# Performance work log

Measured on AMD Instinct MI355X. Metric: run time of the kernel, lower is better.

The kernel has to match this reference:

```python
import jax, jax.numpy as jnp
import numpy as np

N = 100000
E = 1600000
NEG_SLOPE = 0.2


def _param(key, shape, scale=0.05):
    return jax.random.normal(key, shape, dtype=jnp.float32) * scale


def setup_inputs() -> dict:
    key = jax.random.key(0)
    ks = jax.random.split(key, 16)
    x = jax.random.normal(ks[0], (N, 128), dtype=jnp.float32)
    edge_index = jax.random.randint(ks[1], (2, E), 0, N, dtype=jnp.int64)
    # layer 1: 128 -> (H=2, C=64), concat
    W1 = _param(ks[2], (128, 2 * 64)); a_src1 = _param(ks[3], (2, 64)); a_dst1 = _param(ks[4], (2, 64)); b1 = jnp.zeros((128,), jnp.float32)
    # layer 2: 128 -> (H=2, C=64), concat
    W2 = _param(ks[5], (128, 2 * 64)); a_src2 = _param(ks[6], (2, 64)); a_dst2 = _param(ks[7], (2, 64)); b2 = jnp.zeros((128,), jnp.float32)
    # layer 3: 128 -> (H=1, C=64), mean (concat=False)
    W3 = _param(ks[8], (128, 1 * 64)); a_src3 = _param(ks[9], (1, 64)); a_dst3 = _param(ks[10], (1, 64)); b3 = jnp.zeros((64,), jnp.float32)
    return {"x": x, "edge_index": edge_index,
            "W1": W1, "a_src1": a_src1, "a_dst1": a_dst1, "b1": b1,
            "W2": W2, "a_src2": a_src2, "a_dst2": a_dst2, "b2": b2,
            "W3": W3, "a_src3": a_src3, "a_dst3": a_dst3, "b3": b3}


def gat_layer(x, src, dst, W, a_src, a_dst, b, concat):
    H, C = a_src.shape
    n = x.shape[0]
    h = (x @ W).reshape(n, H, C)                      # [N,H,C]
    # per-node attention logits (avoid [E,H,C] gather for the score step)
    al_s = jnp.sum(h * a_src[None], axis=-1)          # [N,H]
    al_d = jnp.sum(h * a_dst[None], axis=-1)          # [N,H]
    e = al_s[src] + al_d[dst]                         # [E',H]
    e = jnp.where(e > 0, e, NEG_SLOPE * e)            # LeakyReLU(0.2)
    # scatter-softmax over incoming edges per destination node
    m = jax.ops.segment_max(e, dst, num_segments=n)   # [N,H]
    ex = jnp.exp(e - m[dst])
    z = jax.ops.segment_sum(ex, dst, num_segments=n)  # [N,H]
    alpha = ex / z[dst]                               # [E',H]
    msg = h[src] * alpha[:, :, None]                  # [E',H,C]
    out = jax.ops.segment_sum(msg, dst, num_segments=n)  # [N,H,C]
    out = out.reshape(n, H * C) if concat else out.mean(axis=1)
    return out + b


def reference(x, edge_index, W1, a_src1, a_dst1, b1, W2, a_src2, a_dst2, b2, W3, a_src3, a_dst3, b3):
    n = x.shape[0]
    loop = jnp.arange(n, dtype=edge_index.dtype)
    src = jnp.concatenate([edge_index[0], loop])      # add self-loops (PyG default)
    dst = jnp.concatenate([edge_index[1], loop])
    h = gat_layer(x, src, dst, W1, a_src1, a_dst1, b1, True)
    h = jax.nn.relu(h)
    h = gat_layer(h, src, dst, W2, a_src2, a_dst2, b2, True)
    h = jax.nn.relu(h)
    return gat_layer(h, src, dst, W3, a_src3, a_dst3, b3, False)
```

## Files before the change

kernel.cpp:

```cpp
#include <hip/hip_runtime.h>
#include <hip/hip_bf16.h>

#define NEG_SLOPE 0.2f
#define BUK_SHIFT 9
#define BUK_SIZE 512
#define BUK_CAP 16384

typedef unsigned short u16;
typedef __attribute__((ext_vector_type(8))) short s8v;
typedef __attribute__((ext_vector_type(4))) float f4v;
typedef _Float16 h8 __attribute__((ext_vector_type(8)));

__device__ __forceinline__ u16 f2bf(float v) {
    unsigned u = __float_as_uint(v);
    unsigned r = u + 0x7FFFu + ((u >> 16) & 1u);
    return (u16)(r >> 16);
}
__device__ __forceinline__ float bf2f(u16 h) { return __uint_as_float(((unsigned)h) << 16); }


__global__ void k_zero(int* g_cnt, int nb) {
    int i = blockIdx.x * blockDim.x + threadIdx.x;
    if (i < nb) g_cnt[i] = 0;
}

__launch_bounds__(256)
__global__ void k_binscatter(const int* __restrict__ ei, int* g_cnt, int* buckets,
                             int E, int nb) {
    __shared__ int lcnt[256], lbase[256], lcur[256];
    int t = threadIdx.x;
    if (t < nb) {
        lcnt[t] = 0;
        lcur[t] = 0;
    }
    __syncthreads();
    int tile0 = blockIdx.x * 4096;
    int pk[16], bk[16];
#pragma unroll
    for (int k = 0; k < 16; k++) {
        int idx = tile0 + k * 256 + t;
        bk[k] = -1;
        if (idx < E) {
            int s = ei[idx];
            int d = ei[E + idx];
            bk[k] = d >> BUK_SHIFT;
            pk[k] = (s << BUK_SHIFT) | (d & (BUK_SIZE - 1));
            atomicAdd(&lcnt[bk[k]], 1);
        }
    }
    __syncthreads();
    if (t < nb && lcnt[t] > 0) lbase[t] = atomicAdd(&g_cnt[t], lcnt[t]);
    __syncthreads();
#pragma unroll
    for (int k = 0; k < 16; k++) {
        if (bk[k] >= 0) {
            int p = lbase[bk[k]] + atomicAdd(&lcur[bk[k]], 1);
            if (p < BUK_CAP) buckets[(bk[k] << 14) + p] = pk[k];
        }
    }
}

__launch_bounds__(512)
__global__ void k_csr(const int* __restrict__ g_cnt, const int* __restrict__ buckets,
                      int* csr_ptr, int* csr_src, int n, int nb) {
    __shared__ int lcnt[512], lsc[512], lcur[512], bsc[512];
    int b = blockIdx.x;
    int t = threadIdx.x;
    int nodes = min(BUK_SIZE, n - b * BUK_SIZE);
    int cnt = min(g_cnt[b], BUK_CAP);
    const int* bp = &buckets[b << 14];

    int bv = 0;
    if (t < nb) bv = min(g_cnt[t], BUK_CAP) + min(BUK_SIZE, n - t * BUK_SIZE);
    bsc[t] = bv;
    __syncthreads();
    for (int off = 1; off < 512; off <<= 1) {
        int x = (t >= off) ? bsc[t - off] : 0;
        __syncthreads();
        bsc[t] += x;
        __syncthreads();
    }
    int boff = bsc[b] - (cnt + nodes);
    int total = bsc[nb - 1];
    __syncthreads();

    lcnt[t] = 0;
    __syncthreads();
    for (int i = t; i < cnt; i += 512) atomicAdd(&lcnt[bp[i] & (BUK_SIZE - 1)], 1);
    __syncthreads();
    int myc = (t < nodes) ? (lcnt[t] + 1) : 0;
    lsc[t] = myc;
    __syncthreads();
    for (int off = 1; off < 512; off <<= 1) {
        int x = (t >= off) ? lsc[t - off] : 0;
        __syncthreads();
        lsc[t] += x;
        __syncthreads();
    }
    int excl = lsc[t] - myc;
    lcur[t] = excl;
    if (t < nodes) csr_ptr[b * BUK_SIZE + t] = boff + excl;
    if (b == nb - 1 && t == 0) csr_ptr[n] = total;
    __syncthreads();
    for (int i = t; i < cnt; i += 512) {
        int v = bp[i];
        int ld = v & (BUK_SIZE - 1);
        int p = atomicAdd(&lcur[ld], 1);
        csr_src[boff + p] = v >> BUK_SHIFT;
    }
    if (t < nodes) {
        int p = atomicAdd(&lcur[t], 1);
        csr_src[boff + p] = b * BUK_SIZE + t;
    }
}


__global__ void k_wsplit_all(const float* __restrict__ W1, const float* __restrict__ W2,
                             const float* __restrict__ W3, u16* __restrict__ T1h,
                             u16* __restrict__ T1l, u16* __restrict__ T2h,
                             u16* __restrict__ T2l, u16* __restrict__ T3h,
                             u16* __restrict__ T3l) {
    int t = blockIdx.x * 256 + threadIdx.x;
    const float* W;
    u16 *Th, *Tl;
    int M, idx;
    if (t < 16384) {
        W = W1; Th = T1h; Tl = T1l; M = 128; idx = t;
    } else if (t < 32768) {
        W = W2; Th = T2h; Tl = T2l; M = 128; idx = t - 16384;
    } else if (t < 40960) {
        W = W3; Th = T3h; Tl = T3l; M = 64; idx = t - 32768;
    } else {
        return;
    }
    int c = idx >> 7, k = idx & 127;
    float v = W[(size_t)k * M + c];
    u16 h = f2bf(v);
    u16 l = f2bf(v - bf2f(h));
    int ct = c >> 4, ch = k >> 5, q = (k >> 3) & 3, j = k & 7;
    size_t addr = ((size_t)ct * 4 + ch) * 512 + ((c & 15) + 16 * q) * 8 + j;
    Th[addr] = h;
    Tl[addr] = l;
}


__device__ __forceinline__ void load_split_f32(const float* __restrict__ X, int row,
                                               int koff, int N, s8v& hi, s8v& lo) {
    float v[8];
    if (row < N) {
        float4 a = *(const float4*)&X[(size_t)row * 128 + koff];
        float4 b = *(const float4*)&X[(size_t)row * 128 + koff + 4];
        v[0] = a.x; v[1] = a.y; v[2] = a.z; v[3] = a.w;
        v[4] = b.x; v[5] = b.y; v[6] = b.z; v[7] = b.w;
    } else {
#pragma unroll
        for (int i = 0; i < 8; i++) v[i] = 0.f;
    }
    union { s8v s; u16 u[8]; } H, L;
#pragma unroll
    for (int i = 0; i < 8; i++) {
        H.u[i] = f2bf(v[i]);
        L.u[i] = f2bf(v[i] - bf2f(H.u[i]));
    }
    hi = H.s;
    lo = L.s;
}

template <int M, bool FP32X>
__launch_bounds__(256)
__global__ void k_gemm_mfma(const float* __restrict__ Xf, const u16* __restrict__ XH,
                            const u16* __restrict__ XL, const u16* __restrict__ WTh,
                            const u16* __restrict__ WTl, const float* __restrict__ asrc,
                            const float* __restrict__ adst, _Float16* __restrict__ Hout,
                            float* __restrict__ als, float* __restrict__ ald, int nrows) {
    const int CT = M / 16;
    const int H = (M == 128) ? 2 : 1;
    int tid = threadIdx.x;
    int wv = tid >> 6, lane = tid & 63;
    int q = lane >> 4, nl = lane & 15;
    int R0 = blockIdx.x * 128 + wv * 32;
    int rt0 = R0 >> 4;

    f4v acc[2][CT];
    f4v z4 = {0.f, 0.f, 0.f, 0.f};
#pragma unroll
    for (int rt = 0; rt < 2; rt++)
#pragma unroll
        for (int ct = 0; ct < CT; ct++) acc[rt][ct] = z4;

#pragma unroll
    for (int ch = 0; ch < 4; ch++) {
        s8v ah0, al0, ah1, al1;
        if (FP32X) {
            int koff = ch * 32 + q * 8;
            load_split_f32(Xf, R0 + nl, koff, nrows, ah0, al0);
            load_split_f32(Xf, R0 + 16 + nl, koff, nrows, ah1, al1);
        } else {
            size_t a0 = ((size_t)rt0 * 4 + ch) * 512 + lane * 8;
            size_t a1 = ((size_t)(rt0 + 1) * 4 + ch) * 512 + lane * 8;
            ah0 = *(const s8v*)&XH[a0];
            al0 = *(const s8v*)&XL[a0];
            ah1 = *(const s8v*)&XH[a1];
            al1 = *(const s8v*)&XL[a1];
        }
#pragma unroll
        for (int ct = 0; ct < CT; ct++) {
            size_t bb = ((size_t)ct * 4 + ch) * 512 + lane * 8;
            s8v bh = *(const s8v*)&WTh[bb];
            s8v bl = *(const s8v*)&WTl[bb];
            acc[0][ct] = __builtin_amdgcn_mfma_f32_16x16x32_bf16(ah0, bh, acc[0][ct], 0, 0, 0);
            acc[0][ct] = __builtin_amdgcn_mfma_f32_16x16x32_bf16(ah0, bl, acc[0][ct], 0, 0, 0);
            acc[0][ct] = __builtin_amdgcn_mfma_f32_16x16x32_bf16(al0, bh, acc[0][ct], 0, 0, 0);
            acc[1][ct] = __builtin_amdgcn_mfma_f32_16x16x32_bf16(ah1, bh, acc[1][ct], 0, 0, 0);
            acc[1][ct] = __builtin_amdgcn_mfma_f32_16x16x32_bf16(ah1, bl, acc[1][ct], 0, 0, 0);
            acc[1][ct] = __builtin_amdgcn_mfma_f32_16x16x32_bf16(al1, bh, acc[1][ct], 0, 0, 0);
        }
    }

    float av[CT], dvv[CT];
#pragma unroll
    for (int ct = 0; ct < CT; ct++) {
        av[ct] = asrc[ct * 16 + nl];
        dvv[ct] = adst[ct * 16 + nl];
    }
    float ps[2][4][2], pd[2][4][2];
#pragma unroll
    for (int rt = 0; rt < 2; rt++)
#pragma unroll
        for (int r = 0; r < 4; r++)
            for (int h = 0; h < 2; h++) ps[rt][r][h] = pd[rt][r][h] = 0.f;
#pragma unroll
    for (int rt = 0; rt < 2; rt++)
#pragma unroll
        for (int ct = 0; ct < CT; ct++) {
            int h = (M == 128) ? (ct >> 2) : 0;
#pragma unroll
            for (int r = 0; r < 4; r++) {
                ps[rt][r][h] = fmaf(acc[rt][ct][r], av[ct], ps[rt][r][h]);
                pd[rt][r][h] = fmaf(acc[rt][ct][r], dvv[ct], pd[rt][r][h]);
            }
        }

#pragma unroll
    for (int rt = 0; rt < 2; rt++)
#pragma unroll
        for (int ct = 0; ct < CT; ct++)
#pragma unroll
            for (int r = 0; r < 4; r++) {
                int row = R0 + rt * 16 + q * 4 + r;
                if (row < nrows) Hout[(size_t)row * M + ct * 16 + nl] = (_Float16)acc[rt][ct][r];
            }

#pragma unroll
    for (int rt = 0; rt < 2; rt++)
#pragma unroll
        for (int r = 0; r < 4; r++)
#pragma unroll
            for (int h = 0; h < H; h++) {
                float v1 = ps[rt][r][h], v2 = pd[rt][r][h];
                for (int m = 1; m <= 8; m <<= 1) {
                    v1 += __shfl_xor(v1, m);
                    v2 += __shfl_xor(v2, m);
                }
                int row = R0 + rt * 16 + q * 4 + r;
                if (nl == 0 && row < nrows) {
                    als[(size_t)row * H + h] = v1;
                    ald[(size_t)row * H + h] = v2;
                }
            }
}


__launch_bounds__(256)
__global__ void k_agg128(const int* __restrict__ ptr, const int* __restrict__ srcv,
                         const _Float16* __restrict__ Hh, const float* __restrict__ als,
                         const float* __restrict__ ald, const float* __restrict__ bias,
                         u16* __restrict__ OutH, u16* __restrict__ OutL, int n) {
    int wid = (blockIdx.x * blockDim.x + threadIdx.x) >> 6;
    int lane = threadIdx.x & 63;
    if (wid >= n) return;
    int start = ptr[wid], end = ptr[wid + 1];
    float2 adv = *(const float2*)&ald[(size_t)wid * 2];
    int grp = lane >> 4;
    int gl = lane & 15;
    int hsel = gl >> 3;
    float z0 = 0.f, z1 = 0.f;
    float acc[8];
#pragma unroll
    for (int c = 0; c < 8; c++) acc[c] = 0.f;

    for (int base = start; base < end; base += 64) {
        int i = base + lane;
        int s_l = 0;
        float ex0 = 0.f, ex1 = 0.f;
        if (i < end) {
            s_l = srcv[i];
            float2 av = *(const float2*)&als[(size_t)s_l * 2];
            float e0 = av.x + adv.x;
            e0 = e0 > 0.f ? e0 : NEG_SLOPE * e0;
            ex0 = __expf(e0);
            float e1 = av.y + adv.y;
            e1 = e1 > 0.f ? e1 : NEG_SLOPE * e1;
            ex1 = __expf(e1);
        }
        z0 += ex0;
        z1 += ex1;
        int cntj = min(64, end - base);
        for (int jp = 0; jp < cntj; jp += 16) {
            int nk = min(4, (cntj - jp + 3) >> 2);
            h8 hv[4];
            float w[4];
#pragma unroll
            for (int k = 0; k < 4; k++) {
                if (k < nk) {
                    int j = jp + 4 * k + grp;
                    int s = __shfl(s_l, j);
                    float w0 = __shfl(ex0, j);
                    float w1 = __shfl(ex1, j);
                    w[k] = hsel ? w1 : w0;
                    hv[k] = *(const h8*)&Hh[(size_t)s * 128 + gl * 8];
                }
            }
#pragma unroll
            for (int k = 0; k < 4; k++) {
                if (k < nk) {
#pragma unroll
                    for (int c = 0; c < 8; c++)
                        acc[c] = fmaf(w[k], (float)hv[k][c], acc[c]);
                }
            }
        }
    }

#pragma unroll
    for (int c = 0; c < 8; c++) {
        acc[c] += __shfl_xor(acc[c], 16);
        acc[c] += __shfl_xor(acc[c], 32);
    }
    for (int m = 32; m >= 1; m >>= 1) {
        z0 += __shfl_xor(z0, m);
        z1 += __shfl_xor(z1, m);
    }
    if (lane < 16) {
        float zinv = hsel ? (1.f / z1) : (1.f / z0);
        int c0 = gl * 8;
        float4 b0 = *(const float4*)&bias[c0];
        float4 b1 = *(const float4*)&bias[c0 + 4];
        float bb[8] = {b0.x, b0.y, b0.z, b0.w, b1.x, b1.y, b1.z, b1.w};
        union { u16 u[8]; s8v v; } HH, LL;
#pragma unroll
        for (int c = 0; c < 8; c++) {
            float o = fmaxf(fmaf(acc[c], zinv, bb[c]), 0.f);
            u16 h = f2bf(o);
            HH.u[c] = h;
            LL.u[c] = f2bf(o - bf2f(h));
        }
        int ch = c0 >> 5, qq = (c0 >> 3) & 3;
        size_t tb = ((size_t)(wid >> 4) * 4 + ch) * 512 + ((size_t)((wid & 15) + 16 * qq)) * 8;
        *(s8v*)&OutH[tb] = HH.v;
        *(s8v*)&OutL[tb] = LL.v;
    }
}


__launch_bounds__(256)
__global__ void k_agg64(const int* __restrict__ ptr, const int* __restrict__ srcv,
                        const _Float16* __restrict__ Hh, const float* __restrict__ als,
                        const float* __restrict__ ald, const float* __restrict__ bias,
                        float* __restrict__ Out, int n) {
    int wid = blockIdx.x * 4 + (threadIdx.x >> 6);
    int lane = threadIdx.x & 63;
    if (wid >= n) return;
    int start = ptr[wid], end = ptr[wid + 1];
    float ad0 = ald[wid];
    int grp = lane >> 3;
    int gl = lane & 7;
    float z = 0.f;
    float acc[8];
#pragma unroll
    for (int c = 0; c < 8; c++) acc[c] = 0.f;

    for (int base = start; base < end; base += 64) {
        int i = base + lane;
        int s_l = 0;
        float ex0 = 0.f;
        if (i < end) {
            s_l = srcv[i];
            float e = als[s_l] + ad0;
            e = e > 0.f ? e : NEG_SLOPE * e;
            ex0 = __expf(e);
        }
        z += ex0;
        int cntj = min(64, end - base);
        for (int jp = 0; jp < cntj; jp += 32) {
            int nk = min(4, (cntj - jp + 7) >> 3);
            h8 hv[4];
            float w[4];
#pragma unroll
            for (int k = 0; k < 4; k++) {
                if (k < nk) {
                    int j = jp + 8 * k + grp;
                    int s = __shfl(s_l, j);
                    w[k] = __shfl(ex0, j);
                    hv[k] = *(const h8*)&Hh[(size_t)s * 64 + gl * 8];
                }
            }
#pragma unroll
            for (int k = 0; k < 4; k++) {
                if (k < nk) {
#pragma unroll
                    for (int c = 0; c < 8; c++)
                        acc[c] = fmaf(w[k], (float)hv[k][c], acc[c]);
                }
            }
        }
    }

#pragma unroll
    for (int c = 0; c < 8; c++) {
        acc[c] += __shfl_xor(acc[c], 8);
        acc[c] += __shfl_xor(acc[c], 16);
        acc[c] += __shfl_xor(acc[c], 32);
    }
    for (int m = 32; m >= 1; m >>= 1) z += __shfl_xor(z, m);
    if (lane < 8) {
        float zinv = 1.f / z;
        int c0 = gl * 8;
        float4 b0 = *(const float4*)&bias[c0];
        float4 b1 = *(const float4*)&bias[c0 + 4];
        float4 o1, o2;
        o1.x = fmaf(acc[0], zinv, b0.x);
        o1.y = fmaf(acc[1], zinv, b0.y);
        o1.z = fmaf(acc[2], zinv, b0.z);
        o1.w = fmaf(acc[3], zinv, b0.w);
        o2.x = fmaf(acc[4], zinv, b1.x);
        o2.y = fmaf(acc[5], zinv, b1.y);
        o2.z = fmaf(acc[6], zinv, b1.z);
        o2.w = fmaf(acc[7], zinv, b1.w);
        *(float4*)&Out[(size_t)wid * 64 + c0] = o1;
        *(float4*)&Out[(size_t)wid * 64 + c0 + 4] = o2;
    }
}


extern "C" void kernel_launch(void* const* d_in, const int* in_sizes, int n_in,
                              void* d_out, int out_size, void* d_ws, size_t ws_size,
                              hipStream_t stream) {
    const float* x = (const float*)d_in[0];
    const int* ei = (const int*)d_in[1];
    const float* W1 = (const float*)d_in[2];
    const float* as1 = (const float*)d_in[3];
    const float* ad1 = (const float*)d_in[4];
    const float* b1 = (const float*)d_in[5];
    const float* W2 = (const float*)d_in[6];
    const float* as2 = (const float*)d_in[7];
    const float* ad2 = (const float*)d_in[8];
    const float* b2 = (const float*)d_in[9];
    const float* W3 = (const float*)d_in[10];
    const float* as3 = (const float*)d_in[11];
    const float* ad3 = (const float*)d_in[12];
    const float* b3 = (const float*)d_in[13];

    const int N = in_sizes[0] / 128;
    const int E = in_sizes[1] / 2;
    const int NB = (N + BUK_SIZE - 1) / BUK_SIZE;
    const int Npad = (N + 127) & ~127;

    char* p = (char*)d_ws;
    auto alloc = [&](size_t bytes) -> char* {
        char* r = p;
        p += (bytes + 255) & ~(size_t)255;
        return r;
    };
    int* g_cnt = (int*)alloc(256 * 4);
    int* buckets = (int*)alloc((size_t)NB * BUK_CAP * 4);
    int* csr_ptr = (int*)alloc((size_t)(N + 1) * 4);
    int* csr_src = (int*)alloc((size_t)(E + N) * 4);
    float* als = (float*)alloc((size_t)N * 2 * 4);
    float* aldv = (float*)alloc((size_t)N * 2 * 4);
    _Float16* Hbuf = (_Float16*)alloc((size_t)N * 128 * 2);
    u16* XH = (u16*)alloc((size_t)Npad * 128 * 2);
    u16* XL = (u16*)alloc((size_t)Npad * 128 * 2);
    u16* WT1h = (u16*)alloc(128 * 128 * 2);
    u16* WT1l = (u16*)alloc(128 * 128 * 2);
    u16* WT2h = (u16*)alloc(128 * 128 * 2);
    u16* WT2l = (u16*)alloc(128 * 128 * 2);
    u16* WT3h = (u16*)alloc(128 * 64 * 2);
    u16* WT3l = (u16*)alloc(128 * 64 * 2);

    const int nbG = Npad / 128;
    const int nbWave = (N * 64 + 255) / 256;
    const int nbAgg64 = (N + 3) / 4;
    const int nbTile = (E + 4095) / 4096;

    k_zero<<<1, 256, 0, stream>>>(g_cnt, 256);
    k_binscatter<<<nbTile, 256, 0, stream>>>(ei, g_cnt, buckets, E, NB);
    k_csr<<<NB, 512, 0, stream>>>(g_cnt, buckets, csr_ptr, csr_src, N, NB);

    k_wsplit_all<<<160, 256, 0, stream>>>(W1, W2, W3, WT1h, WT1l, WT2h, WT2l, WT3h, WT3l);

    k_gemm_mfma<128, true><<<nbG, 256, 0, stream>>>(x, nullptr, nullptr, WT1h, WT1l,
                                                    as1, ad1, Hbuf, als, aldv, N);
    k_agg128<<<nbWave, 256, 0, stream>>>(csr_ptr, csr_src, Hbuf, als, aldv, b1, XH, XL, N);

    k_gemm_mfma<128, false><<<nbG, 256, 0, stream>>>(nullptr, XH, XL, WT2h, WT2l,
                                                     as2, ad2, Hbuf, als, aldv, N);
    k_agg128<<<nbWave, 256, 0, stream>>>(csr_ptr, csr_src, Hbuf, als, aldv, b2, XH, XL, N);

    k_gemm_mfma<64, false><<<nbG, 256, 0, stream>>>(nullptr, XH, XL, WT3h, WT3l,
                                                    as3, ad3, Hbuf, als, aldv, N);
    k_agg64<<<nbAgg64, 256, 0, stream>>>(csr_ptr, csr_src, Hbuf, als, aldv, b3,
                                         (float*)d_out, N);
}
```

Before: 448.9 us.

## Switch split GEMM to fp16 MFMA and store hidden activations as single fp16

Replaces the bf16 hi/lo split with an fp16 hi/lo split for weights and the first-layer input, using f16 MFMA instructions. Intermediate activations written by the 128-wide aggregation are stored as a single fp16 tensor instead of a hi/lo pair, so layers 2 and 3 read half the activation bytes and issue four MFMAs per tile instead of six. The aggregation kernels also widen their gather batch to eight neighbour rows per step for more memory-level parallelism. The trade-off is lower precision for intermediate activations (fp16 range and mantissa) and higher register use in the aggregation loops.

```diff
diff --git a/kernel.cpp b/kernel.cpp
--- a/kernel.cpp
+++ b/kernel.cpp
@@ -7,16 +7,14 @@
 #define BUK_CAP 16384
 
 typedef unsigned short u16;
-typedef __attribute__((ext_vector_type(8))) short s8v;
 typedef __attribute__((ext_vector_type(4))) float f4v;
 typedef _Float16 h8 __attribute__((ext_vector_type(8)));
 
-__device__ __forceinline__ u16 f2bf(float v) {
-    unsigned u = __float_as_uint(v);
-    unsigned r = u + 0x7FFFu + ((u >> 16) & 1u);
-    return (u16)(r >> 16);
-}
-__device__ __forceinline__ float bf2f(u16 h) { return __uint_as_float(((unsigned)h) << 16); }
+__device__ __forceinline__ u16 f2h_bits(_Float16 h) {
+    union { _Float16 f; u16 u; } c;
+    c.f = h;
+    return c.u;
+}
 
 
 __global__ void k_zero(int* g_cnt, int nb) {
@@ -135,17 +133,17 @@
     }
     int c = idx >> 7, k = idx & 127;
     float v = W[(size_t)k * M + c];
-    u16 h = f2bf(v);
-    u16 l = f2bf(v - bf2f(h));
+    _Float16 h = (_Float16)v;
+    _Float16 l = (_Float16)(v - (float)h);
     int ct = c >> 4, ch = k >> 5, q = (k >> 3) & 3, j = k & 7;
     size_t addr = ((size_t)ct * 4 + ch) * 512 + ((c & 15) + 16 * q) * 8 + j;
-    Th[addr] = h;
-    Tl[addr] = l;
+    Th[addr] = f2h_bits(h);
+    Tl[addr] = f2h_bits(l);
 }
 
 
 __device__ __forceinline__ void load_split_f32(const float* __restrict__ X, int row,
-                                               int koff, int N, s8v& hi, s8v& lo) {
+                                               int koff, int N, h8& hi, h8& lo) {
     float v[8];
     if (row < N) {
         float4 a = *(const float4*)&X[(size_t)row * 128 + koff];
@@ -156,11 +154,11 @@
 #pragma unroll
         for (int i = 0; i < 8; i++) v[i] = 0.f;
     }
-    union { s8v s; u16 u[8]; } H, L;
+    union { h8 s; _Float16 u[8]; } H, L;
 #pragma unroll
     for (int i = 0; i < 8; i++) {
-        H.u[i] = f2bf(v[i]);
-        L.u[i] = f2bf(v[i] - bf2f(H.u[i]));
+        H.u[i] = (_Float16)v[i];
+        L.u[i] = (_Float16)(v[i] - (float)H.u[i]);
     }
     hi = H.s;
     lo = L.s;
@@ -169,10 +167,10 @@
 template <int M, bool FP32X>
 __launch_bounds__(256)
 __global__ void k_gemm_mfma(const float* __restrict__ Xf, const u16* __restrict__ XH,
-                            const u16* __restrict__ XL, const u16* __restrict__ WTh,
-                            const u16* __restrict__ WTl, const float* __restrict__ asrc,
-                            const float* __restrict__ adst, _Float16* __restrict__ Hout,
-                            float* __restrict__ als, float* __restrict__ ald, int nrows) {
+                            const u16* __restrict__ WTh, const u16* __restrict__ WTl,
+                            const float* __restrict__ asrc, const float* __restrict__ adst,
+                            _Float16* __restrict__ Hout, float* __restrict__ als,
+                            float* __restrict__ ald, int nrows) {
     const int CT = M / 16;
     const int H = (M == 128) ? 2 : 1;
     int tid = threadIdx.x;
@@ -190,7 +188,7 @@
 
 #pragma unroll
     for (int ch = 0; ch < 4; ch++) {
-        s8v ah0, al0, ah1, al1;
+        h8 ah0, al0, ah1, al1;
         if (FP32X) {
             int koff = ch * 32 + q * 8;
             load_split_f32(Xf, R0 + nl, koff, nrows, ah0, al0);
@@ -198,22 +196,22 @@
         } else {
             size_t a0 = ((size_t)rt0 * 4 + ch) * 512 + lane * 8;
             size_t a1 = ((size_t)(rt0 + 1) * 4 + ch) * 512 + lane * 8;
-            ah0 = *(const s8v*)&XH[a0];
-            al0 = *(const s8v*)&XL[a0];
-            ah1 = *(const s8v*)&XH[a1];
-            al1 = *(const s8v*)&XL[a1];
+            ah0 = *(const h8*)&XH[a0];
+            ah1 = *(const h8*)&XH[a1];
         }
 #pragma unroll
         for (int ct = 0; ct < CT; ct++) {
             size_t bb = ((size_t)ct * 4 + ch) * 512 + lane * 8;
-            s8v bh = *(const s8v*)&WTh[bb];
-            s8v bl = *(const s8v*)&WTl[bb];
-            acc[0][ct] = __builtin_amdgcn_mfma_f32_16x16x32_bf16(ah0, bh, acc[0][ct], 0, 0, 0);
-            acc[0][ct] = __builtin_amdgcn_mfma_f32_16x16x32_bf16(ah0, bl, acc[0][ct], 0, 0, 0);
-            acc[0][ct] = __builtin_amdgcn_mfma_f32_16x16x32_bf16(al0, bh, acc[0][ct], 0, 0, 0);
-            acc[1][ct] = __builtin_amdgcn_mfma_f32_16x16x32_bf16(ah1, bh, acc[1][ct], 0, 0, 0);
-            acc[1][ct] = __builtin_amdgcn_mfma_f32_16x16x32_bf16(ah1, bl, acc[1][ct], 0, 0, 0);
-            acc[1][ct] = __builtin_amdgcn_mfma_f32_16x16x32_bf16(al1, bh, acc[1][ct], 0, 0, 0);
+            h8 bh = *(const h8*)&WTh[bb];
+            h8 bl = *(const h8*)&WTl[bb];
+            acc[0][ct] = __builtin_amdgcn_mfma_f32_16x16x32_f16(ah0, bh, acc[0][ct], 0, 0, 0);
+            acc[0][ct] = __builtin_amdgcn_mfma_f32_16x16x32_f16(ah0, bl, acc[0][ct], 0, 0, 0);
+            acc[1][ct] = __builtin_amdgcn_mfma_f32_16x16x32_f16(ah1, bh, acc[1][ct], 0, 0, 0);
+            acc[1][ct] = __builtin_amdgcn_mfma_f32_16x16x32_f16(ah1, bl, acc[1][ct], 0, 0, 0);
+            if (FP32X) {
+                acc[0][ct] = __builtin_amdgcn_mfma_f32_16x16x32_f16(al0, bh, acc[0][ct], 0, 0, 0);
+                acc[1][ct] = __builtin_amdgcn_mfma_f32_16x16x32_f16(al1, bh, acc[1][ct], 0, 0, 0);
+            }
         }
     }
 
@@ -275,7 +273,7 @@
 __global__ void k_agg128(const int* __restrict__ ptr, const int* __restrict__ srcv,
                          const _Float16* __restrict__ Hh, const float* __restrict__ als,
                          const float* __restrict__ ald, const float* __restrict__ bias,
-                         u16* __restrict__ OutH, u16* __restrict__ OutL, int n) {
+                         u16* __restrict__ OutX, int n) {
     int wid = (blockIdx.x * blockDim.x + threadIdx.x) >> 6;
     int lane = threadIdx.x & 63;
     if (wid >= n) return;
@@ -306,12 +304,12 @@
         z0 += ex0;
         z1 += ex1;
         int cntj = min(64, end - base);
-        for (int jp = 0; jp < cntj; jp += 16) {
-            int nk = min(4, (cntj - jp + 3) >> 2);
-            h8 hv[4];
-            float w[4];
-#pragma unroll
-            for (int k = 0; k < 4; k++) {
+        for (int jp = 0; jp < cntj; jp += 32) {
+            int nk = min(8, (cntj - jp + 3) >> 2);
+            h8 hv[8];
+            float w[8];
+#pragma unroll
+            for (int k = 0; k < 8; k++) {
                 if (k < nk) {
                     int j = jp + 4 * k + grp;
                     int s = __shfl(s_l, j);
@@ -322,7 +320,7 @@
                 }
             }
 #pragma unroll
-            for (int k = 0; k < 4; k++) {
+            for (int k = 0; k < 8; k++) {
                 if (k < nk) {
 #pragma unroll
                     for (int c = 0; c < 8; c++)
@@ -347,18 +345,15 @@
         float4 b0 = *(const float4*)&bias[c0];
         float4 b1 = *(const float4*)&bias[c0 + 4];
         float bb[8] = {b0.x, b0.y, b0.z, b0.w, b1.x, b1.y, b1.z, b1.w};
-        union { u16 u[8]; s8v v; } HH, LL;
+        union { _Float16 f[8]; h8 v; } O;
 #pragma unroll
         for (int c = 0; c < 8; c++) {
             float o = fmaxf(fmaf(acc[c], zinv, bb[c]), 0.f);
-            u16 h = f2bf(o);
-            HH.u[c] = h;
-            LL.u[c] = f2bf(o - bf2f(h));
+            O.f[c] = (_Float16)o;
         }
         int ch = c0 >> 5, qq = (c0 >> 3) & 3;
         size_t tb = ((size_t)(wid >> 4) * 4 + ch) * 512 + ((size_t)((wid & 15) + 16 * qq)) * 8;
-        *(s8v*)&OutH[tb] = HH.v;
-        *(s8v*)&OutL[tb] = LL.v;
+        *(h8*)&OutX[tb] = O.v;
     }
 }
 
@@ -392,26 +387,24 @@
         }
         z += ex0;
         int cntj = min(64, end - base);
-        for (int jp = 0; jp < cntj; jp += 32) {
-            int nk = min(4, (cntj - jp + 7) >> 3);
-            h8 hv[4];
-            float w[4];
-#pragma unroll
-            for (int k = 0; k < 4; k++) {
-                if (k < nk) {
-                    int j = jp + 8 * k + grp;
-                    int s = __shfl(s_l, j);
-                    w[k] = __shfl(ex0, j);
-                    hv[k] = *(const h8*)&Hh[(size_t)s * 64 + gl * 8];
-                }
-            }
-#pragma unroll
-            for (int k = 0; k < 4; k++) {
-                if (k < nk) {
-#pragma unroll
-                    for (int c = 0; c < 8; c++)
-                        acc[c] = fmaf(w[k], (float)hv[k][c], acc[c]);
-                }
+        int nk = (cntj + 7) >> 3;
+        h8 hv[8];
+        float w[8];
+#pragma unroll
+        for (int k = 0; k < 8; k++) {
+            if (k < nk) {
+                int j = 8 * k + grp;
+                int s = __shfl(s_l, j);
+                w[k] = __shfl(ex0, j);
+                hv[k] = *(const h8*)&Hh[(size_t)s * 64 + gl * 8];
+            }
+        }
+#pragma unroll
+        for (int k = 0; k < 8; k++) {
+            if (k < nk) {
+#pragma unroll
+                for (int c = 0; c < 8; c++)
+                    acc[c] = fmaf(w[k], (float)hv[k][c], acc[c]);
             }
         }
     }
@@ -480,7 +473,6 @@
     float* aldv = (float*)alloc((size_t)N * 2 * 4);
     _Float16* Hbuf = (_Float16*)alloc((size_t)N * 128 * 2);
     u16* XH = (u16*)alloc((size_t)Npad * 128 * 2);
-    u16* XL = (u16*)alloc((size_t)Npad * 128 * 2);
     u16* WT1h = (u16*)alloc(128 * 128 * 2);
     u16* WT1l = (u16*)alloc(128 * 128 * 2);
     u16* WT2h = (u16*)alloc(128 * 128 * 2);
@@ -499,15 +491,15 @@
 
     k_wsplit_all<<<160, 256, 0, stream>>>(W1, W2, W3, WT1h, WT1l, WT2h, WT2l, WT3h, WT3l);
 
-    k_gemm_mfma<128, true><<<nbG, 256, 0, stream>>>(x, nullptr, nullptr, WT1h, WT1l,
+    k_gemm_mfma<128, true><<<nbG, 256, 0, stream>>>(x, nullptr, WT1h, WT1l,
                                                     as1, ad1, Hbuf, als, aldv, N);
-    k_agg128<<<nbWave, 256, 0, stream>>>(csr_ptr, csr_src, Hbuf, als, aldv, b1, XH, XL, N);
-
-    k_gemm_mfma<128, false><<<nbG, 256, 0, stream>>>(nullptr, XH, XL, WT2h, WT2l,
+    k_agg128<<<nbWave, 256, 0, stream>>>(csr_ptr, csr_src, Hbuf, als, aldv, b1, XH, N);
+
+    k_gemm_mfma<128, false><<<nbG, 256, 0, stream>>>(nullptr, XH, WT2h, WT2l,
                                                      as2, ad2, Hbuf, als, aldv, N);
-    k_agg128<<<nbWave, 256, 0, stream>>>(csr_ptr, csr_src, Hbuf, als, aldv, b2, XH, XL, N);
-
-    k_gemm_mfma<64, false><<<nbG, 256, 0, stream>>>(nullptr, XH, XL, WT3h, WT3l,
+    k_agg128<<<nbWave, 256, 0, stream>>>(csr_ptr, csr_src, Hbuf, als, aldv, b2, XH, N);
+
+    k_gemm_mfma<64, false><<<nbG, 256, 0, stream>>>(nullptr, XH, WT3h, WT3l,
                                                     as3, ad3, Hbuf, als, aldv, N);
     k_agg64<<<nbAgg64, 256, 0, stream>>>(csr_ptr, csr_src, Hbuf, als, aldv, b3,
                                          (float*)d_out, N);
```

Measured after the change: 453.3 us. Within noise of the previous version (+1.0%).
